# Kernel optimization log

Hardware: AMD Instinct MI355X
Metric: run time of the kernel (lower is better)

## Reference

```python
import jax, jax.numpy as jnp
import numpy as np

BN_EPS = 1e-3      # Keras BatchNormalization default epsilon
LRELU_ALPHA = 0.3  # Keras LeakyReLU default alpha


def _bn(x, gamma, beta, mean, var):
    # inference-mode batch norm over the feature (last) axis
    return gamma * (x - mean) * jax.lax.rsqrt(var + BN_EPS) + beta


def _gcn(x, adj, w, b):
    # spektral GCNConv: A_hat @ (X @ W) + b   (adj assumed pre-normalized)
    xw = jnp.einsum('bnf,fc->bnc', x, w)
    return jnp.einsum('bnm,bmc->bnc', adj, xw) + b


def _lrelu(x):
    return jnp.where(x >= 0, x, LRELU_ALPHA * x)


def setup_inputs() -> dict:
    key = jax.random.key(0)
    ks = jax.random.split(key, 12)
    B, N, C = 16, 1024, 256
    x = jax.random.normal(ks[0], (B, N, C), dtype=jnp.float32)
    # roughly row-normalized dense adjacency (stands in for D^-1/2 (A+I) D^-1/2)
    adj = jax.random.uniform(ks[1], (B, N, N), dtype=jnp.float32) / N
    s = 1.0 / np.sqrt(C)
    return {
        'x': x,
        'adj': adj,
        'bn1_gamma': jnp.ones((C,), jnp.float32),
        'bn1_beta': jnp.zeros((C,), jnp.float32),
        'bn1_mean': jax.random.normal(ks[2], (C,), jnp.float32) * 0.1,
        'bn1_var': jax.random.uniform(ks[3], (C,), jnp.float32) + 0.5,
        'w1': jax.random.normal(ks[4], (C, C), jnp.float32) * s,
        'b1': jnp.zeros((C,), jnp.float32),
        'bn2_gamma': jnp.ones((C,), jnp.float32),
        'bn2_beta': jnp.zeros((C,), jnp.float32),
        'bn2_mean': jax.random.normal(ks[5], (C,), jnp.float32) * 0.1,
        'bn2_var': jax.random.uniform(ks[6], (C,), jnp.float32) + 0.5,
        'w2': jax.random.normal(ks[7], (C, C), jnp.float32) * s,
        'b2': jnp.zeros((C,), jnp.float32),
        'w_skip': jax.random.normal(ks[8], (C, C), jnp.float32) * s,
        'b_skip': jnp.zeros((C,), jnp.float32),
    }


def reference(x, adj, bn1_gamma, bn1_beta, bn1_mean, bn1_var, w1, b1,
              bn2_gamma, bn2_beta, bn2_mean, bn2_var, w2, b2, w_skip, b_skip):
    h = _bn(x, bn1_gamma, bn1_beta, bn1_mean, bn1_var)          # BN(input)
    out = _lrelu(_gcn(h, adj, w1, b1))                          # GCNConv + LeakyReLU
    out = _bn(out, bn2_gamma, bn2_beta, bn2_mean, bn2_var)      # BN
    out = _lrelu(_gcn(out, adj, w2, b2))                        # GCNConv + LeakyReLU
    skip = _gcn(h, adj, w_skip, b_skip)                         # skip GCNConv on BN(input)
    # Dropout is identity at inference
    return out + skip
```

## Files before the change

kernel.cpp:

```cpp
#include <hip/hip_runtime.h>

#define LRELU_ALPHA 0.3f
#define BN_EPS 1e-3f

using u16 = unsigned short;
using u32 = unsigned int;

typedef __attribute__((ext_vector_type(8))) short bf16x8;
typedef __attribute__((ext_vector_type(4))) float f32x4;

struct alignas(8) U16x4 { u16 x, y, z, w; };

__device__ __forceinline__ u16 f2bf(float f) {
  union { float f; u32 u; } v; v.f = f;
  u32 b = v.u;
  b += 0x7FFFu + ((b >> 16) & 1u);
  return (u16)(b >> 16);
}
__device__ __forceinline__ float bf2f(u16 h) {
  union { u32 u; float f; } v; v.u = ((u32)h) << 16;
  return v.f;
}

typedef const __attribute__((address_space(1))) void* gas_ptr;
typedef __attribute__((address_space(3))) void* las_ptr;

__device__ __forceinline__ void gload16(const void* g, void* l) {
  __builtin_amdgcn_global_load_lds((gas_ptr)g, (las_ptr)l, 16, 0, 0);
}

template <int K>
__device__ __forceinline__ void gemm_core(const u16* __restrict__ A,
                                          const u16* __restrict__ B,
                                          u16* lds,
                                          f32x4 (&acc)[4][4]) {
  const int t    = threadIdx.x;
  const int lane = t & 63;
  const int wid  = t >> 6;
  const int wm   = (wid >> 1) * 64;
  const int wn   = (wid & 1) * 64;
  const int lrow = lane & 15;
  const int lk   = (lane >> 4) * 8;

  const int r0 = t >> 3;
  const int ce = (t & 7) * 8;
  const int lo = (t >> 6) * 512;

  auto stage = [&](int buf, int kt) {
    u16* ldsA = lds + buf * 16384;
    u16* ldsB = ldsA + 8192;
    const u16* gA = A + kt * 64;
    const u16* gB = B + kt * 64;
#pragma unroll
    for (int cc = 0; cc < 4; ++cc) {
      gload16(gA + (size_t)(cc * 32 + r0) * K + ce, ldsA + cc * 2048 + lo);
      gload16(gB + (size_t)(cc * 32 + r0) * K + ce, ldsB + cc * 2048 + lo);
    }
  };

  auto compute = [&](int buf) {
    const u16* As = lds + buf * 16384;
    const u16* Bs = As + 8192;
#pragma unroll
    for (int kk = 0; kk < 2; ++kk) {
      bf16x8 a[4], b[4];
#pragma unroll
      for (int i = 0; i < 4; ++i)
        a[i] = *(const bf16x8*)(As + (wm + i * 16 + lrow) * 64 + kk * 32 + lk);
#pragma unroll
      for (int i = 0; i < 4; ++i)
        b[i] = *(const bf16x8*)(Bs + (wn + i * 16 + lrow) * 64 + kk * 32 + lk);
#pragma unroll
      for (int i = 0; i < 4; ++i)
#pragma unroll
        for (int j = 0; j < 4; ++j)
          acc[i][j] = __builtin_amdgcn_mfma_f32_16x16x32_bf16(a[i], b[j], acc[i][j], 0, 0, 0);
    }
  };

  const int KT = K / 64;
  stage(0, 0);
  asm volatile("s_waitcnt vmcnt(0)" ::: "memory");
  __syncthreads();
  int cur = 0;
#pragma unroll 1
  for (int kt = 0; kt < KT - 1; ++kt) {
    stage(cur ^ 1, kt + 1);
    compute(cur);
    asm volatile("s_waitcnt vmcnt(0)" ::: "memory");
    __syncthreads();
    cur ^= 1;
  }
  compute(cur);
}

#define ACC_INIT()                                  \
  f32x4 acc[4][4];                                  \
  _Pragma("unroll") for (int i_ = 0; i_ < 4; ++i_)  \
  _Pragma("unroll") for (int j_ = 0; j_ < 4; ++j_)  \
      acc[i_][j_] = {0.f, 0.f, 0.f, 0.f};

#define EPI_COORDS()                                          \
  const int t = threadIdx.x, lane = t & 63, wid = t >> 6;     \
  const int row0 = (wid >> 1) * 64 + (lane >> 4) * 4;         \
  const int col0 = (wid & 1) * 64 + (lane & 15);

__global__ void k_prep(const float* __restrict__ w1, const float* __restrict__ wsk,
                       const float* __restrict__ w2,
                       const float* __restrict__ g1, const float* __restrict__ be1,
                       const float* __restrict__ m1, const float* __restrict__ v1,
                       const float* __restrict__ g2, const float* __restrict__ be2,
                       const float* __restrict__ m2, const float* __restrict__ v2,
                       u16* __restrict__ wcatT, u16* __restrict__ w2T,
                       float* __restrict__ s1, float* __restrict__ t1,
                       float* __restrict__ s2, float* __restrict__ t2c) {
  if (blockIdx.x == 0) {
    int c = threadIdx.x;
    float a1 = g1[c] * rsqrtf(v1[c] + BN_EPS);
    s1[c] = a1; t1[c] = be1[c] - m1[c] * a1;
    float a2 = g2[c] * rsqrtf(v2[c] + BN_EPS);
    s2[c] = a2; t2c[c] = be2[c] - m2[c] * a2;
  }
  int i = blockIdx.x * 256 + threadIdx.x;
  if (i < 131072) {
    int co = i >> 8, ci = i & 255;
    const float* w = (co < 256) ? w1 : wsk;
    wcatT[i] = f2bf(w[ci * 256 + (co & 255)]);
  } else if (i < 196608) {
    int k = i - 131072;
    int co = k >> 8, ci = k & 255;
    w2T[k] = f2bf(w2[ci * 256 + co]);
  }
}

__global__ void k_convert(const float* __restrict__ adj, const float* __restrict__ x,
                          const float* __restrict__ s1, const float* __restrict__ t1,
                          u16* __restrict__ adj_bf, u16* __restrict__ h_bf) {
  const int NA = 4194304;
  const int NH = 1048576;
  int stride = gridDim.x * blockDim.x;
  for (int idx = blockIdx.x * blockDim.x + threadIdx.x; idx < NA + NH; idx += stride) {
    if (idx < NA) {
      float4 v = ((const float4*)adj)[idx];
      U16x4 o = {f2bf(v.x), f2bf(v.y), f2bf(v.z), f2bf(v.w)};
      ((U16x4*)adj_bf)[idx] = o;
    } else {
      int k = idx - NA;
      float4 v = ((const float4*)x)[k];
      int c = (k << 2) & 255;
      U16x4 o = {f2bf(v.x * s1[c] + t1[c]),         f2bf(v.y * s1[c + 1] + t1[c + 1]),
                 f2bf(v.z * s1[c + 2] + t1[c + 2]), f2bf(v.w * s1[c + 3] + t1[c + 3])};
      ((U16x4*)h_bf)[k] = o;
    }
  }
}

__global__ __launch_bounds__(256) void k_xw(const u16* __restrict__ h_bf,
                                            const u16* __restrict__ wcatT,
                                            u16* __restrict__ hwT) {
  __shared__ u16 lds[32768];
  ACC_INIT();
  const int mt = blockIdx.x, nt = blockIdx.y;
  gemm_core<256>(h_bf + (size_t)mt * 128 * 256, wcatT + (size_t)nt * 128 * 256, lds, acc);

  EPI_COORDS();
  __syncthreads();
  u16* tl = lds;
#pragma unroll
  for (int j = 0; j < 4; ++j) {
    int co_l = col0 + j * 16;
#pragma unroll
    for (int i = 0; i < 4; ++i)
#pragma unroll
      for (int r = 0; r < 4; ++r)
        tl[co_l * 136 + row0 + i * 16 + r] = f2bf(acc[i][j][r]);
  }
  __syncthreads();
  const int rw = t >> 4, seg = t & 15;
  const int b = mt >> 3, nb = (mt & 7) * 128;
#pragma unroll
  for (int p = 0; p < 8; ++p) {
    int co_l = p * 16 + rw;
    *(bf16x8*)(hwT + (((size_t)(b * 512 + nt * 128 + co_l)) << 10) + nb + seg * 8) =
        *(const bf16x8*)(tl + co_l * 136 + seg * 8);
  }
}

__global__ __launch_bounds__(256) void k_big1(const u16* __restrict__ adj_bf,
                                              const u16* __restrict__ hwT,
                                              const float* __restrict__ b1,
                                              const float* __restrict__ bsk,
                                              const float* __restrict__ s2,
                                              const float* __restrict__ t2c,
                                              u16* __restrict__ u2b,
                                              u16* __restrict__ skipb) {
  __shared__ u16 lds[32768];
  ACC_INIT();
  const int mt = blockIdx.x, nt = blockIdx.y, bz = blockIdx.z;
  gemm_core<1024>(adj_bf + ((size_t)bz << 20) + (size_t)mt * 128 * 1024,
                  hwT    + ((size_t)bz << 19) + (size_t)nt * 128 * 1024, lds, acc);

  EPI_COORDS();
  const bool conv = (nt < 2);
  const int cb = (nt & 1) * 128;
  __syncthreads();
  u16* tl = lds;
#pragma unroll
  for (int j = 0; j < 4; ++j) {
    int cl = col0 + j * 16;
    int c = cb + cl;
    float bias = conv ? b1[c] : bsk[c];
    float sc = s2[c], tc = t2c[c];
#pragma unroll
    for (int i = 0; i < 4; ++i)
#pragma unroll
      for (int r = 0; r < 4; ++r) {
        float y = acc[i][j][r] + bias;
        float v;
        if (conv) {
          float u = (y >= 0.f) ? y : LRELU_ALPHA * y;
          v = fmaf(u, sc, tc);
        } else {
          v = y;
        }
        tl[(row0 + i * 16 + r) * 136 + cl] = f2bf(v);
      }
  }
  __syncthreads();
  u16* dstbase = (conv ? u2b : skipb) + ((size_t)bz << 18) + cb;
  const int rw = t >> 4, seg = t & 15;
  const int nb = mt * 128;
#pragma unroll
  for (int p = 0; p < 8; ++p) {
    int nl = p * 16 + rw;
    *(bf16x8*)(dstbase + ((size_t)(nb + nl) << 8) + seg * 8) =
        *(const bf16x8*)(tl + nl * 136 + seg * 8);
  }
}

__global__ __launch_bounds__(256) void k_sm2(const u16* __restrict__ w2T,
                                             const u16* __restrict__ u2b,
                                             u16* __restrict__ t2T) {
  __shared__ u16 lds[32768];
  ACC_INIT();
  const int mt = blockIdx.x, nt = blockIdx.y, bz = blockIdx.z;
  gemm_core<256>(w2T + (size_t)mt * 128 * 256,
                 u2b + ((size_t)bz << 18) + (size_t)nt * 128 * 256, lds, acc);

  EPI_COORDS();
  __syncthreads();
  u16* tl = lds;
#pragma unroll
  for (int j = 0; j < 4; ++j) {
    int nl = col0 + j * 16;
#pragma unroll
    for (int i = 0; i < 4; ++i)
#pragma unroll
      for (int r = 0; r < 4; ++r)
        tl[(row0 + i * 16 + r) * 136 + nl] = f2bf(acc[i][j][r]);
  }
  __syncthreads();
  const int rw = t >> 4, seg = t & 15;
  u16* base = t2T + ((size_t)bz << 18) + nt * 128;
#pragma unroll
  for (int p = 0; p < 8; ++p) {
    int co_l = p * 16 + rw;
    *(bf16x8*)(base + (((size_t)(mt * 128 + co_l)) << 10) + seg * 8) =
        *(const bf16x8*)(tl + co_l * 136 + seg * 8);
  }
}

__global__ __launch_bounds__(256) void k_big2(const u16* __restrict__ adj_bf,
                                              const u16* __restrict__ t2T,
                                              const float* __restrict__ b2,
                                              const u16* __restrict__ skipb,
                                              float* __restrict__ outp) {
  __shared__ u16 lds[32768];
  ACC_INIT();
  const int mt = blockIdx.x, nt = blockIdx.y, bz = blockIdx.z;
  gemm_core<1024>(adj_bf + ((size_t)bz << 20) + (size_t)mt * 128 * 1024,
                  t2T    + ((size_t)bz << 18) + (size_t)nt * 128 * 1024, lds, acc);

  EPI_COORDS();
  __syncthreads();
  float* tf = (float*)lds;
#pragma unroll
  for (int j = 0; j < 4; ++j) {
    int cl = col0 + j * 16;
    float bias = b2[nt * 128 + cl];
#pragma unroll
    for (int i = 0; i < 4; ++i)
#pragma unroll
      for (int r = 0; r < 4; ++r) {
        float y = acc[i][j][r] + bias;
        tf[(row0 + i * 16 + r) * 128 + cl] = (y >= 0.f) ? y : LRELU_ALPHA * y;
      }
  }
  __syncthreads();
  const int rw = t >> 5, seg = t & 31;
  const int cbase = nt * 128;
#pragma unroll
  for (int p = 0; p < 16; ++p) {
    int nl = p * 8 + rw;
    size_t go = ((size_t)bz << 18) + ((size_t)(mt * 128 + nl) << 8) + cbase + seg * 4;
    float4 v = *(const float4*)(tf + nl * 128 + seg * 4);
    U16x4 sk = *(const U16x4*)(skipb + go);
    float4 o = {v.x + bf2f(sk.x), v.y + bf2f(sk.y), v.z + bf2f(sk.z), v.w + bf2f(sk.w)};
    *(float4*)(outp + go) = o;
  }
}

extern "C" void kernel_launch(void* const* d_in, const int* in_sizes, int n_in,
                              void* d_out, int out_size, void* d_ws, size_t ws_size,
                              hipStream_t stream) {
  const float* x   = (const float*)d_in[0];
  const float* adj = (const float*)d_in[1];
  const float* g1  = (const float*)d_in[2];
  const float* be1 = (const float*)d_in[3];
  const float* mu1 = (const float*)d_in[4];
  const float* v1  = (const float*)d_in[5];
  const float* w1  = (const float*)d_in[6];
  const float* b1  = (const float*)d_in[7];
  const float* g2  = (const float*)d_in[8];
  const float* be2 = (const float*)d_in[9];
  const float* mu2 = (const float*)d_in[10];
  const float* v2  = (const float*)d_in[11];
  const float* w2  = (const float*)d_in[12];
  const float* b2  = (const float*)d_in[13];
  const float* wsk = (const float*)d_in[14];
  const float* bsk = (const float*)d_in[15];
  float* out = (float*)d_out;

  char* ws = (char*)d_ws;
  u16*   adj_bf = (u16*)(ws);
  u16*   hwT    = (u16*)(ws + 33554432);
  u16*   h_bf   = (u16*)(ws + 50331648);
  u16*   u2b    = (u16*)(ws + 58720256);
  u16*   t2T    = (u16*)(ws + 67108864);
  u16*   skipb  = (u16*)(ws + 75497472);
  u16*   wcatT  = (u16*)(ws + 83886080);
  u16*   w2T    = (u16*)(ws + 84148224);
  float* s1     = (float*)(ws + 84279296);
  float* t1     = (float*)(ws + 84280320);
  float* s2     = (float*)(ws + 84281344);
  float* t2c    = (float*)(ws + 84282368);
  if (ws_size < 84283392) return;

  k_prep   <<<768, 256, 0, stream>>>(w1, wsk, w2, g1, be1, mu1, v1, g2, be2, mu2, v2,
                                     wcatT, w2T, s1, t1, s2, t2c);
  k_convert<<<2048, 256, 0, stream>>>(adj, x, s1, t1, adj_bf, h_bf);
  k_xw  <<<dim3(128, 4),   256, 0, stream>>>(h_bf, wcatT, hwT);
  k_big1<<<dim3(8, 4, 16), 256, 0, stream>>>(adj_bf, hwT, b1, bsk, s2, t2c, u2b, skipb);
  k_sm2 <<<dim3(2, 8, 16), 256, 0, stream>>>(w2T, u2b, t2T);
  k_big2<<<dim3(8, 2, 16), 256, 0, stream>>>(adj_bf, t2T, b2, skipb, out);
}
```

Measured before the change: 216.9 us.

## Single-buffer GEMM core, fuse prep kernels, add 128x64 tiles for small grids

Drops LDS double-buffering in the GEMM core so each block uses less shared memory and more blocks can be resident per CU. BN1 and the x conversion move into the weight-prep kernel, and the adj fp32-to-bf16 conversion runs as extra blocks inside the X@W kernel, cutting the launch count. k_sm2 and k_big2 now use 128x64 tiles, doubling their grid to fill more CUs. The trade-off is that load latency is no longer overlapped with compute inside a block and now depends on occupancy across blocks.

Result: slower. 242.2 us (+11.7%).

```diff
diff --git a/kernel.cpp b/kernel.cpp
--- a/kernel.cpp
+++ b/kernel.cpp
@@ -32,23 +32,15 @@
 template <int K>
 __device__ __forceinline__ void gemm_core(const u16* __restrict__ A,
                                           const u16* __restrict__ B,
-                                          u16* lds,
-                                          f32x4 (&acc)[4][4]) {
-  const int t    = threadIdx.x;
-  const int lane = t & 63;
-  const int wid  = t >> 6;
-  const int wm   = (wid >> 1) * 64;
-  const int wn   = (wid & 1) * 64;
-  const int lrow = lane & 15;
-  const int lk   = (lane >> 4) * 8;
-
-  const int r0 = t >> 3;
-  const int ce = (t & 7) * 8;
-  const int lo = (t >> 6) * 512;
-
-  auto stage = [&](int buf, int kt) {
-    u16* ldsA = lds + buf * 16384;
-    u16* ldsB = ldsA + 8192;
+                                          u16* lds, f32x4 (&acc)[4][4]) {
+  const int t = threadIdx.x, lane = t & 63, wid = t >> 6;
+  const int wm = (wid >> 1) * 64, wn = (wid & 1) * 64;
+  const int lrow = lane & 15, lk = (lane >> 4) * 8;
+  const int r0 = t >> 3, ce = (t & 7) * 8, lo = wid * 512;
+  u16* ldsA = lds;
+  u16* ldsB = lds + 8192;
+#pragma unroll 1
+  for (int kt = 0; kt < K / 64; ++kt) {
     const u16* gA = A + kt * 64;
     const u16* gB = B + kt * 64;
 #pragma unroll
@@ -56,114 +48,149 @@
       gload16(gA + (size_t)(cc * 32 + r0) * K + ce, ldsA + cc * 2048 + lo);
       gload16(gB + (size_t)(cc * 32 + r0) * K + ce, ldsB + cc * 2048 + lo);
     }
-  };
-
-  auto compute = [&](int buf) {
-    const u16* As = lds + buf * 16384;
-    const u16* Bs = As + 8192;
+    asm volatile("s_waitcnt vmcnt(0)" ::: "memory");
+    __syncthreads();
 #pragma unroll
     for (int kk = 0; kk < 2; ++kk) {
       bf16x8 a[4], b[4];
 #pragma unroll
       for (int i = 0; i < 4; ++i)
-        a[i] = *(const bf16x8*)(As + (wm + i * 16 + lrow) * 64 + kk * 32 + lk);
+        a[i] = *(const bf16x8*)(ldsA + (wm + i * 16 + lrow) * 64 + kk * 32 + lk);
 #pragma unroll
       for (int i = 0; i < 4; ++i)
-        b[i] = *(const bf16x8*)(Bs + (wn + i * 16 + lrow) * 64 + kk * 32 + lk);
+        b[i] = *(const bf16x8*)(ldsB + (wn + i * 16 + lrow) * 64 + kk * 32 + lk);
 #pragma unroll
       for (int i = 0; i < 4; ++i)
 #pragma unroll
         for (int j = 0; j < 4; ++j)
           acc[i][j] = __builtin_amdgcn_mfma_f32_16x16x32_bf16(a[i], b[j], acc[i][j], 0, 0, 0);
     }
-  };
-
-  const int KT = K / 64;
-  stage(0, 0);
-  asm volatile("s_waitcnt vmcnt(0)" ::: "memory");
-  __syncthreads();
-  int cur = 0;
+    __syncthreads();
+  }
+}
+
+template <int K>
+__device__ __forceinline__ void gemm_core64(const u16* __restrict__ A,
+                                            const u16* __restrict__ B,
+                                            u16* lds, f32x4 (&acc)[2][4]) {
+  const int t = threadIdx.x, lane = t & 63, wid = t >> 6;
+  const int wm = wid * 32;
+  const int lrow = lane & 15, lk = (lane >> 4) * 8;
+  const int r0 = t >> 3, ce = (t & 7) * 8, lo = wid * 512;
+  u16* ldsA = lds;
+  u16* ldsB = lds + 8192;
 #pragma unroll 1
-  for (int kt = 0; kt < KT - 1; ++kt) {
-    stage(cur ^ 1, kt + 1);
-    compute(cur);
+  for (int kt = 0; kt < K / 64; ++kt) {
+    const u16* gA = A + kt * 64;
+    const u16* gB = B + kt * 64;
+#pragma unroll
+    for (int cc = 0; cc < 4; ++cc)
+      gload16(gA + (size_t)(cc * 32 + r0) * K + ce, ldsA + cc * 2048 + lo);
+#pragma unroll
+    for (int cc = 0; cc < 2; ++cc)
+      gload16(gB + (size_t)(cc * 32 + r0) * K + ce, ldsB + cc * 2048 + lo);
     asm volatile("s_waitcnt vmcnt(0)" ::: "memory");
     __syncthreads();
-    cur ^= 1;
-  }
-  compute(cur);
-}
-
-#define ACC_INIT()                                  \
-  f32x4 acc[4][4];                                  \
-  _Pragma("unroll") for (int i_ = 0; i_ < 4; ++i_)  \
+#pragma unroll
+    for (int kk = 0; kk < 2; ++kk) {
+      bf16x8 a[2], b[4];
+#pragma unroll
+      for (int i = 0; i < 2; ++i)
+        a[i] = *(const bf16x8*)(ldsA + (wm + i * 16 + lrow) * 64 + kk * 32 + lk);
+#pragma unroll
+      for (int j = 0; j < 4; ++j)
+        b[j] = *(const bf16x8*)(ldsB + (j * 16 + lrow) * 64 + kk * 32 + lk);
+#pragma unroll
+      for (int i = 0; i < 2; ++i)
+#pragma unroll
+        for (int j = 0; j < 4; ++j)
+          acc[i][j] = __builtin_amdgcn_mfma_f32_16x16x32_bf16(a[i], b[j], acc[i][j], 0, 0, 0);
+    }
+    __syncthreads();
+  }
+}
+
+#define ACC_INIT(R)                                 \
+  f32x4 acc[R][4];                                  \
+  _Pragma("unroll") for (int i_ = 0; i_ < R; ++i_)  \
   _Pragma("unroll") for (int j_ = 0; j_ < 4; ++j_)  \
       acc[i_][j_] = {0.f, 0.f, 0.f, 0.f};
 
-#define EPI_COORDS()                                          \
-  const int t = threadIdx.x, lane = t & 63, wid = t >> 6;     \
-  const int row0 = (wid >> 1) * 64 + (lane >> 4) * 4;         \
+__global__ __launch_bounds__(256) void k_prep_h(
+    const float* __restrict__ w1, const float* __restrict__ wsk, const float* __restrict__ w2,
+    const float* __restrict__ g1, const float* __restrict__ be1,
+    const float* __restrict__ m1, const float* __restrict__ v1,
+    const float* __restrict__ g2, const float* __restrict__ be2,
+    const float* __restrict__ m2, const float* __restrict__ v2,
+    const float* __restrict__ x,
+    u16* __restrict__ wcatT, u16* __restrict__ w2T,
+    float* __restrict__ s2, float* __restrict__ t2c, u16* __restrict__ h_bf) {
+  int bid = blockIdx.x;
+  if (bid < 768) {
+    if (bid == 0) {
+      int c = threadIdx.x;
+      float a2 = g2[c] * rsqrtf(v2[c] + BN_EPS);
+      s2[c] = a2;
+      t2c[c] = be2[c] - m2[c] * a2;
+    }
+    int i = bid * 256 + threadIdx.x;
+    if (i < 131072) {
+      int co = i >> 8, ci = i & 255;
+      const float* w = (co < 256) ? w1 : wsk;
+      wcatT[i] = f2bf(w[ci * 256 + (co & 255)]);
+    } else {
+      int k = i - 131072;
+      int co = k >> 8, ci = k & 255;
+      w2T[k] = f2bf(w2[ci * 256 + co]);
+    }
+  } else {
+    int base = (bid - 768) * 256 + threadIdx.x;
+    int c0 = (base << 2) & 255;
+    float sc[4], sh[4];
+#pragma unroll
+    for (int u = 0; u < 4; ++u) {
+      int c = c0 + u;
+      float a = g1[c] * rsqrtf(v1[c] + BN_EPS);
+      sc[u] = a;
+      sh[u] = be1[c] - m1[c] * a;
+    }
+#pragma unroll
+    for (int j = 0; j < 16; ++j) {
+      int k = j * 65536 + base;
+      float4 v = ((const float4*)x)[k];
+      U16x4 o = {f2bf(v.x * sc[0] + sh[0]), f2bf(v.y * sc[1] + sh[1]),
+                 f2bf(v.z * sc[2] + sh[2]), f2bf(v.w * sc[3] + sh[3])};
+      ((U16x4*)h_bf)[k] = o;
+    }
+  }
+}
+
+__global__ __launch_bounds__(256) void k_xw_cvt(const float* __restrict__ adj,
+                                                u16* __restrict__ adj_bf,
+                                                const u16* __restrict__ h_bf,
+                                                const u16* __restrict__ wcatT,
+                                                u16* __restrict__ hwT) {
+  __shared__ u16 lds[17408];
+  const int bid = blockIdx.x;
+  const int r = bid % 5;
+  if (r == 4) {
+    const int stripe = bid / 5;
+    const float4* src = (const float4*)adj + (size_t)stripe * 32768;
+    U16x4* dst = (U16x4*)adj_bf + (size_t)stripe * 32768;
+    for (int i = threadIdx.x; i < 32768; i += 256) {
+      float4 v = src[i];
+      U16x4 o = {f2bf(v.x), f2bf(v.y), f2bf(v.z), f2bf(v.w)};
+      dst[i] = o;
+    }
+    return;
+  }
+  const int mt = bid / 5, nt = r;
+  ACC_INIT(4);
+  gemm_core<256>(h_bf + (size_t)mt * 128 * 256, wcatT + (size_t)nt * 128 * 256, lds, acc);
+
+  const int t = threadIdx.x, lane = t & 63, wid = t >> 6;
+  const int row0 = (wid >> 1) * 64 + (lane >> 4) * 4;
   const int col0 = (wid & 1) * 64 + (lane & 15);
-
-__global__ void k_prep(const float* __restrict__ w1, const float* __restrict__ wsk,
-                       const float* __restrict__ w2,
-                       const float* __restrict__ g1, const float* __restrict__ be1,
-                       const float* __restrict__ m1, const float* __restrict__ v1,
-                       const float* __restrict__ g2, const float* __restrict__ be2,
-                       const float* __restrict__ m2, const float* __restrict__ v2,
-                       u16* __restrict__ wcatT, u16* __restrict__ w2T,
-                       float* __restrict__ s1, float* __restrict__ t1,
-                       float* __restrict__ s2, float* __restrict__ t2c) {
-  if (blockIdx.x == 0) {
-    int c = threadIdx.x;
-    float a1 = g1[c] * rsqrtf(v1[c] + BN_EPS);
-    s1[c] = a1; t1[c] = be1[c] - m1[c] * a1;
-    float a2 = g2[c] * rsqrtf(v2[c] + BN_EPS);
-    s2[c] = a2; t2c[c] = be2[c] - m2[c] * a2;
-  }
-  int i = blockIdx.x * 256 + threadIdx.x;
-  if (i < 131072) {
-    int co = i >> 8, ci = i & 255;
-    const float* w = (co < 256) ? w1 : wsk;
-    wcatT[i] = f2bf(w[ci * 256 + (co & 255)]);
-  } else if (i < 196608) {
-    int k = i - 131072;
-    int co = k >> 8, ci = k & 255;
-    w2T[k] = f2bf(w2[ci * 256 + co]);
-  }
-}
-
-__global__ void k_convert(const float* __restrict__ adj, const float* __restrict__ x,
-                          const float* __restrict__ s1, const float* __restrict__ t1,
-                          u16* __restrict__ adj_bf, u16* __restrict__ h_bf) {
-  const int NA = 4194304;
-  const int NH = 1048576;
-  int stride = gridDim.x * blockDim.x;
-  for (int idx = blockIdx.x * blockDim.x + threadIdx.x; idx < NA + NH; idx += stride) {
-    if (idx < NA) {
-      float4 v = ((const float4*)adj)[idx];
-      U16x4 o = {f2bf(v.x), f2bf(v.y), f2bf(v.z), f2bf(v.w)};
-      ((U16x4*)adj_bf)[idx] = o;
-    } else {
-      int k = idx - NA;
-      float4 v = ((const float4*)x)[k];
-      int c = (k << 2) & 255;
-      U16x4 o = {f2bf(v.x * s1[c] + t1[c]),         f2bf(v.y * s1[c + 1] + t1[c + 1]),
-                 f2bf(v.z * s1[c + 2] + t1[c + 2]), f2bf(v.w * s1[c + 3] + t1[c + 3])};
-      ((U16x4*)h_bf)[k] = o;
-    }
-  }
-}
-
-__global__ __launch_bounds__(256) void k_xw(const u16* __restrict__ h_bf,
-                                            const u16* __restrict__ wcatT,
-                                            u16* __restrict__ hwT) {
-  __shared__ u16 lds[32768];
-  ACC_INIT();
-  const int mt = blockIdx.x, nt = blockIdx.y;
-  gemm_core<256>(h_bf + (size_t)mt * 128 * 256, wcatT + (size_t)nt * 128 * 256, lds, acc);
-
-  EPI_COORDS();
   __syncthreads();
   u16* tl = lds;
 #pragma unroll
@@ -172,8 +199,8 @@
 #pragma unroll
     for (int i = 0; i < 4; ++i)
 #pragma unroll
-      for (int r = 0; r < 4; ++r)
-        tl[co_l * 136 + row0 + i * 16 + r] = f2bf(acc[i][j][r]);
+      for (int q = 0; q < 4; ++q)
+        tl[co_l * 136 + row0 + i * 16 + q] = f2bf(acc[i][j][q]);
   }
   __syncthreads();
   const int rw = t >> 4, seg = t & 15;
@@ -194,13 +221,15 @@
                                               const float* __restrict__ t2c,
                                               u16* __restrict__ u2b,
                                               u16* __restrict__ skipb) {
-  __shared__ u16 lds[32768];
-  ACC_INIT();
+  __shared__ u16 lds[17408];
+  ACC_INIT(4);
   const int mt = blockIdx.x, nt = blockIdx.y, bz = blockIdx.z;
   gemm_core<1024>(adj_bf + ((size_t)bz << 20) + (size_t)mt * 128 * 1024,
                   hwT    + ((size_t)bz << 19) + (size_t)nt * 128 * 1024, lds, acc);
 
-  EPI_COORDS();
+  const int t = threadIdx.x, lane = t & 63, wid = t >> 6;
+  const int row0 = (wid >> 1) * 64 + (lane >> 4) * 4;
+  const int col0 = (wid & 1) * 64 + (lane & 15);
   const bool conv = (nt < 2);
   const int cb = (nt & 1) * 128;
   __syncthreads();
@@ -214,8 +243,8 @@
 #pragma unroll
     for (int i = 0; i < 4; ++i)
 #pragma unroll
-      for (int r = 0; r < 4; ++r) {
-        float y = acc[i][j][r] + bias;
+      for (int q = 0; q < 4; ++q) {
+        float y = acc[i][j][q] + bias;
         float v;
         if (conv) {
           float u = (y >= 0.f) ? y : LRELU_ALPHA * y;
@@ -223,7 +252,7 @@
         } else {
           v = y;
         }
-        tl[(row0 + i * 16 + r) * 136 + cl] = f2bf(v);
+        tl[(row0 + i * 16 + q) * 136 + cl] = f2bf(v);
       }
   }
   __syncthreads();
@@ -241,32 +270,32 @@
 __global__ __launch_bounds__(256) void k_sm2(const u16* __restrict__ w2T,
                                              const u16* __restrict__ u2b,
                                              u16* __restrict__ t2T) {
-  __shared__ u16 lds[32768];
-  ACC_INIT();
+  __shared__ u16 lds[12288];
+  ACC_INIT(2);
   const int mt = blockIdx.x, nt = blockIdx.y, bz = blockIdx.z;
-  gemm_core<256>(w2T + (size_t)mt * 128 * 256,
-                 u2b + ((size_t)bz << 18) + (size_t)nt * 128 * 256, lds, acc);
-
-  EPI_COORDS();
+  gemm_core64<256>(w2T + (size_t)mt * 128 * 256,
+                   u2b + ((size_t)bz << 18) + (size_t)nt * 64 * 256, lds, acc);
+
+  const int t = threadIdx.x, lane = t & 63, wid = t >> 6;
+  const int row0 = wid * 32 + (lane >> 4) * 4;
+  const int col0 = lane & 15;
   __syncthreads();
   u16* tl = lds;
 #pragma unroll
-  for (int j = 0; j < 4; ++j) {
-    int nl = col0 + j * 16;
-#pragma unroll
-    for (int i = 0; i < 4; ++i)
-#pragma unroll
-      for (int r = 0; r < 4; ++r)
-        tl[(row0 + i * 16 + r) * 136 + nl] = f2bf(acc[i][j][r]);
-  }
-  __syncthreads();
-  const int rw = t >> 4, seg = t & 15;
-  u16* base = t2T + ((size_t)bz << 18) + nt * 128;
-#pragma unroll
-  for (int p = 0; p < 8; ++p) {
-    int co_l = p * 16 + rw;
-    *(bf16x8*)(base + (((size_t)(mt * 128 + co_l)) << 10) + seg * 8) =
-        *(const bf16x8*)(tl + co_l * 136 + seg * 8);
+  for (int j = 0; j < 4; ++j)
+#pragma unroll
+    for (int i = 0; i < 2; ++i)
+#pragma unroll
+      for (int q = 0; q < 4; ++q)
+        tl[(row0 + i * 16 + q) * 72 + col0 + j * 16] = f2bf(acc[i][j][q]);
+  __syncthreads();
+  u16* base = t2T + ((size_t)bz << 18) + nt * 64;
+  const int rw = t >> 3, seg = t & 7;
+#pragma unroll
+  for (int p = 0; p < 4; ++p) {
+    int co = p * 32 + rw;
+    *(bf16x8*)(base + (((size_t)(mt * 128 + co)) << 10) + seg * 8) =
+        *(const bf16x8*)(tl + co * 72 + seg * 8);
   }
 }
 
@@ -275,35 +304,36 @@
                                               const float* __restrict__ b2,
                                               const u16* __restrict__ skipb,
                                               float* __restrict__ outp) {
-  __shared__ u16 lds[32768];
-  ACC_INIT();
+  __shared__ u16 lds[17408];
+  ACC_INIT(2);
   const int mt = blockIdx.x, nt = blockIdx.y, bz = blockIdx.z;
-  gemm_core<1024>(adj_bf + ((size_t)bz << 20) + (size_t)mt * 128 * 1024,
-                  t2T    + ((size_t)bz << 18) + (size_t)nt * 128 * 1024, lds, acc);
-
-  EPI_COORDS();
+  gemm_core64<1024>(adj_bf + ((size_t)bz << 20) + (size_t)mt * 128 * 1024,
+                    t2T    + ((size_t)bz << 18) + (size_t)nt * 64 * 1024, lds, acc);
+
+  const int t = threadIdx.x, lane = t & 63, wid = t >> 6;
+  const int row0 = wid * 32 + (lane >> 4) * 4;
+  const int col0 = lane & 15;
   __syncthreads();
   float* tf = (float*)lds;
 #pragma unroll
   for (int j = 0; j < 4; ++j) {
     int cl = col0 + j * 16;
-    float bias = b2[nt * 128 + cl];
-#pragma unroll
-    for (int i = 0; i < 4; ++i)
-#pragma unroll
-      for (int r = 0; r < 4; ++r) {
-        float y = acc[i][j][r] + bias;
-        tf[(row0 + i * 16 + r) * 128 + cl] = (y >= 0.f) ? y : LRELU_ALPHA * y;
+    float bias = b2[nt * 64 + cl];
+#pragma unroll
+    for (int i = 0; i < 2; ++i)
+#pragma unroll
+      for (int q = 0; q < 4; ++q) {
+        float y = acc[i][j][q] + bias;
+        tf[(row0 + i * 16 + q) * 68 + cl] = (y >= 0.f) ? y : LRELU_ALPHA * y;
       }
   }
   __syncthreads();
-  const int rw = t >> 5, seg = t & 31;
-  const int cbase = nt * 128;
-#pragma unroll
-  for (int p = 0; p < 16; ++p) {
-    int nl = p * 8 + rw;
-    size_t go = ((size_t)bz << 18) + ((size_t)(mt * 128 + nl) << 8) + cbase + seg * 4;
-    float4 v = *(const float4*)(tf + nl * 128 + seg * 4);
+  const int rw = t >> 4, seg = t & 15;
+#pragma unroll
+  for (int p = 0; p < 8; ++p) {
+    int nl = p * 16 + rw;
+    size_t go = ((size_t)bz << 18) + ((size_t)(mt * 128 + nl) << 8) + nt * 64 + seg * 4;
+    float4 v = *(const float4*)(tf + nl * 68 + seg * 4);
     U16x4 sk = *(const U16x4*)(skipb + go);
     float4 o = {v.x + bf2f(sk.x), v.y + bf2f(sk.y), v.z + bf2f(sk.z), v.w + bf2f(sk.w)};
     *(float4*)(outp + go) = o;
@@ -340,17 +370,14 @@
   u16*   skipb  = (u16*)(ws + 75497472);
   u16*   wcatT  = (u16*)(ws + 83886080);
   u16*   w2T    = (u16*)(ws + 84148224);
-  float* s1     = (float*)(ws + 84279296);
-  float* t1     = (float*)(ws + 84280320);
   float* s2     = (float*)(ws + 84281344);
   float* t2c    = (float*)(ws + 84282368);
   if (ws_size < 84283392) return;
 
-  k_prep   <<<768, 256, 0, stream>>>(w1, wsk, w2, g1, be1, mu1, v1, g2, be2, mu2, v2,
-                                     wcatT, w2T, s1, t1, s2, t2c);
-  k_convert<<<2048, 256, 0, stream>>>(adj, x, s1, t1, adj_bf, h_bf);
-  k_xw  <<<dim3(128, 4),   256, 0, stream>>>(h_bf, wcatT, hwT);
-  k_big1<<<dim3(8, 4, 16), 256, 0, stream>>>(adj_bf, hwT, b1, bsk, s2, t2c, u2b, skipb);
-  k_sm2 <<<dim3(2, 8, 16), 256, 0, stream>>>(w2T, u2b, t2T);
-  k_big2<<<dim3(8, 2, 16), 256, 0, stream>>>(adj_bf, t2T, b2, skipb, out);
-}
+  k_prep_h <<<1024, 256, 0, stream>>>(w1, wsk, w2, g1, be1, mu1, v1, g2, be2, mu2, v2,
+                                      x, wcatT, w2T, s2, t2c, h_bf);
+  k_xw_cvt <<<640, 256, 0, stream>>>(adj, adj_bf, h_bf, wcatT, hwT);
+  k_big1<<<dim3(8, 4, 16),  256, 0, stream>>>(adj_bf, hwT, b1, bsk, s2, t2c, u2b, skipb);
+  k_sm2 <<<dim3(2, 16, 16), 256, 0, stream>>>(w2T, u2b, t2T);
+  k_big2<<<dim3(8, 4, 16),  256, 0, stream>>>(adj_bf, t2T, b2, skipb, out);
+}
```
